# Optimization experiments

Measured on AMD Instinct MI355X. Metric: run time of the kernel, lower is better.

Reference implementation:

```python
import jax, jax.numpy as jnp
import numpy as np

STRIDE = 1
PAD = 1
KH = KW = 3


def _conv2d(x, w, b, stride, pad):
    out = jax.lax.conv_general_dilated(
        x, w, window_strides=(stride, stride),
        padding=[(pad, pad), (pad, pad)],
        dimension_numbers=("NCHW", "OIHW", "NCHW"))
    return out + b[None, :, None, None]


def _deform_conv2d(x, offset, mask, weight, stride, pad):
    """Modulated deformable conv v2 (torchvision deform_conv2d semantics, no bias).

    x: [B,C,H,W]  offset: [B,2*K2,Ho,Wo] (dy,dx interleaved per tap)
    mask: [B,K2,Ho,Wo]  weight: [O,C,KH,KW]
    """
    B, C, H, W = x.shape
    O = weight.shape[0]
    K2 = KH * KW
    Ho, Wo = offset.shape[2], offset.shape[3]

    dy = offset[:, 0::2]  # [B,K2,Ho,Wo]
    dx = offset[:, 1::2]

    # base sampling grid per kernel tap k = i*KW + j
    ki = jnp.repeat(jnp.arange(KH), KW)  # [K2]
    kj = jnp.tile(jnp.arange(KW), KH)    # [K2]
    base_y = (jnp.arange(Ho) * stride - pad)[None, :, None] + ki[:, None, None]  # [K2,Ho,1]
    base_x = (jnp.arange(Wo) * stride - pad)[None, None, :] + kj[:, None, None]  # [K2,1,Wo]

    py = base_y[None].astype(x.dtype) + dy  # [B,K2,Ho,Wo]
    px = base_x[None].astype(x.dtype) + dx

    y0f = jnp.floor(py)
    x0f = jnp.floor(px)
    wy = py - y0f  # bilinear weights
    wx = px - x0f
    y0 = y0f.astype(jnp.int32)
    x0 = x0f.astype(jnp.int32)

    x_flat = x.reshape(B, C, H * W)

    def gather(yi, xi):
        # zero padding: out-of-range integer neighbors contribute 0
        valid = (yi >= 0) & (yi < H) & (xi >= 0) & (xi < W)
        idx = jnp.clip(yi, 0, H - 1) * W + jnp.clip(xi, 0, W - 1)  # [B,K2,Ho,Wo]
        g = jax.vmap(lambda xf, id_: xf[:, id_])(x_flat, idx)      # [B,C,K2,Ho,Wo]
        return g * valid[:, None].astype(x.dtype)

    v00 = gather(y0, x0)
    v01 = gather(y0, x0 + 1)
    v10 = gather(y0 + 1, x0)
    v11 = gather(y0 + 1, x0 + 1)

    wy_ = wy[:, None]  # [B,1,K2,Ho,Wo]
    wx_ = wx[:, None]
    val = (v00 * (1 - wy_) * (1 - wx_) + v01 * (1 - wy_) * wx_
           + v10 * wy_ * (1 - wx_) + v11 * wy_ * wx_)
    val = val * mask[:, None]

    # conv accumulation over (C, K2)
    return jnp.einsum("bckhw,ock->bohw", val, weight.reshape(O, C, K2))


def setup_inputs() -> dict:
    key = jax.random.key(0)
    ks = jax.random.split(key, 6)
    B, C, O, H, W = 4, 128, 128, 64, 64
    x = jax.random.normal(ks[0], (B, C, H, W), dtype=jnp.float32)
    org_w = jax.random.normal(ks[1], (O, C, KH, KW), dtype=jnp.float32) * 0.05
    offset_w = jax.random.normal(ks[2], (2 * KH * KW, C, 3, 3), dtype=jnp.float32) * 0.01
    offset_b = jax.random.normal(ks[3], (2 * KH * KW,), dtype=jnp.float32) * 0.01
    mask_w = jax.random.normal(ks[4], (KH * KW, C, 3, 3), dtype=jnp.float32) * 0.01
    mask_b = jax.random.normal(ks[5], (KH * KW,), dtype=jnp.float32) * 0.01
    return {"x": x, "org_w": org_w, "offset_w": offset_w, "offset_b": offset_b,
            "mask_w": mask_w, "mask_b": mask_b}


def reference(x, org_w, offset_w, offset_b, mask_w, mask_b):
    offset = _conv2d(x, offset_w, offset_b, STRIDE, 1)          # [B,18,H,W]
    mask = jax.nn.sigmoid(_conv2d(x, mask_w, mask_b, STRIDE, 1))  # [B,9,H,W]
    return _deform_conv2d(x, offset, mask, org_w, STRIDE, PAD)
```

## Files before the change

kernel.cpp:

```cpp
#include <hip/hip_runtime.h>
#include <hip/hip_bf16.h>
#include <cmath>

#define B_    4
#define C_    128
#define O_    128
#define K2T   9
#define CK    1152
#define NPIX  4096
#define ROWS  8
#define BUFC  512
#define BUFF  8192
#define NGRP  36

using bf16   = __bf16;
using bf16x8 = __attribute__((ext_vector_type(8))) __bf16;
using f32x4  = __attribute__((ext_vector_type(4))) float;

#define WS_WBF 0
#define WS_WOM 294912

__global__ void __launch_bounds__(256) repack_kernel(
    const float* __restrict__ org_w, const float* __restrict__ offset_w,
    const float* __restrict__ mask_w, bf16* __restrict__ w_bf,
    bf16* __restrict__ wom_bf) {
  int t = blockIdx.x * 256 + threadIdx.x;
  if (t >= 160 * CK) return;
  int row = t / CK, r = t % CK;
  int cc = r / 288, rr = r % 288;
  int k = rr >> 5, cq = rr & 31;
  int c = cc * 32 + cq;
  if (row < 128) {
    w_bf[t] = (bf16)org_w[((size_t)row * C_ + c) * K2T + k];
  } else {
    int ch = row - 128;
    float v = 0.f;
    if (ch < 18)      v = offset_w[((size_t)ch * C_ + c) * K2T + k];
    else if (ch < 27) v = mask_w[((size_t)(ch - 18) * C_ + c) * K2T + k];
    wom_bf[(size_t)ch * CK + r] = (bf16)v;
  }
}

__device__ __forceinline__ void gl_lds16(const float* src, float* lds_uniform) {
  __builtin_amdgcn_global_load_lds(
      (const __attribute__((address_space(1))) void*)src,
      (__attribute__((address_space(3))) void*)lds_uniform, 16, 0, 0);
}

__global__ void __launch_bounds__(576) deform_fused_kernel(
    const float* __restrict__ x, const bf16* __restrict__ w_bf,
    const bf16* __restrict__ wom_bf, const float* __restrict__ off_b,
    const float* __restrict__ mask_b, float* __restrict__ out) {
  __shared__ __align__(16) float xslab[3 * BUFF];
  __shared__ __align__(16) bf16  valbuf[NGRP * 512];
  __shared__ __align__(16) float S_lds[32 * 64];

  int tid  = threadIdx.x;
  int bid0 = blockIdx.x;
  int bid  = (bid0 & 7) * 32 + (bid0 >> 3);
  int b    = bid >> 6, ho = bid & 63;
  int lane = tid & 63, wv = tid >> 6;
  int l15  = lane & 15, l4 = lane >> 4;
  bool w8  = (wv < 8);

  const float* xb = x + (size_t)b * C_ * NPIX;

  auto stage = [&](int it2) {
    if (w8 && it2 < 16) {
      int ccs = (it2 & 7) >> 1, g2s = it2 & 1;
      float* dstb = xslab + (it2 % 3) * BUFF;
#pragma unroll
      for (int u = 0; u < 2; ++u) {
        int chl = 2 * wv + u;
        int ch  = ccs * 32 + g2s * 16 + chl;
        const float* srcb = xb + (size_t)ch * NPIX + l15 * 4;
        float* dst = dstb + chl * BUFC;
#pragma unroll
        for (int j = 0; j < 2; ++j) {
          int y = ho - 3 + j * 4 + l4;
          y = y < 0 ? 0 : (y > 63 ? 63 : y);
          gl_lds16(srcb + y * 64, dst + j * 256);
        }
      }
    }
  };

  float apw; int apsa;
  {
    int k = wv, p = lane;
    int ki = k / 3, kj = k % 3;
    int row = ho - 1 + ki, colu = p - 1 + kj;
    bool ok = ((unsigned)row < 64u) && ((unsigned)colu < 64u);
    int cc0 = colu < 0 ? 0 : (colu > 63 ? 63 : colu);
    apw  = ok ? 1.f : 0.f;
    apsa = (ki + 2) * 64 + cc0;
  }

  stage(0);
  stage(1);
  __builtin_amdgcn_sched_barrier(0);

  f32x4 acc1 = {};
  f32x4 acc[4] = {};
  bf16x8 aF[9];
  float pw0 = 0.f, pw1 = 0.f, pw2 = 0.f, pw3 = 0.f;
  int   psa = 0, psb = 0;
  int   mf = wv & 1, nfq = wv >> 1;
  const bf16* wbase1 = wom_bf + (size_t)(mf * 16 + l15) * CK + l4 * 8;
  const bf16* wbase  = w_bf  + (size_t)(wv * 16 + l15) * CK + l4 * 8;
  const bf16* vb1    = valbuf + l4 * 512 + (nfq * 16 + l15) * 8;
  const bf16* vbase  = valbuf + l4 * 512 + l15 * 8;

#pragma unroll 1
  for (int hp = 0; hp < 16; ++hp) {
    int c2 = hp >> 1;
    bool passB = (c2 >= 4);
    int cc = c2 & 3;
    if (hp == 15) asm volatile("s_waitcnt vmcnt(0)" ::: "memory");
    else          asm volatile("s_waitcnt vmcnt(4)" ::: "memory");
    __builtin_amdgcn_s_barrier();
    __builtin_amdgcn_sched_barrier(0);
    if (!(hp & 1) && w8) {
      const bf16* ab = (passB ? wbase : wbase1) + cc * 288;
#pragma unroll
      for (int ks = 0; ks < 9; ++ks) aF[ks] = *(const bf16x8*)(ab + ks * 32);
      __builtin_amdgcn_sched_barrier(0);
    }
    stage(hp + 2);
    __builtin_amdgcn_sched_barrier(0);
    {
      const float* sbuf = xslab + (hp % 3) * BUFF;
      int grp = wv * 4 + (hp & 1) * 2;
      if (passB) {
#pragma unroll
        for (int h = 0; h < 2; ++h) {
          bf16x8 pack;
#pragma unroll
          for (int j = 0; j < 8; ++j) {
            const float* cb = sbuf + (h * 8 + j) * BUFC;
            float a0 = cb[psa], a1 = cb[psa + 64];
            float b0 = cb[psb], b1 = cb[psb + 64];
            pack[j] = (bf16)(pw0 * a0 + pw1 * b0 + pw2 * a1 + pw3 * b1);
          }
          *(bf16x8*)(valbuf + (grp + h) * 512 + lane * 8) = pack;
        }
      } else {
#pragma unroll
        for (int h = 0; h < 2; ++h) {
          bf16x8 pack;
#pragma unroll
          for (int j = 0; j < 8; ++j)
            pack[j] = (bf16)(apw * sbuf[(h * 8 + j) * BUFC + apsa]);
          *(bf16x8*)(valbuf + (grp + h) * 512 + lane * 8) = pack;
        }
      }
    }
    if (hp & 1) {
      asm volatile("s_waitcnt lgkmcnt(0)" ::: "memory");
      __builtin_amdgcn_s_barrier();
      __builtin_amdgcn_sched_barrier(0);
      if (w8) {
        __builtin_amdgcn_s_setprio(1);
        if (passB) {
#pragma unroll
          for (int ks = 0; ks < 9; ++ks) {
#pragma unroll
            for (int nf = 0; nf < 4; ++nf) {
              bf16x8 bv = *(const bf16x8*)(vbase + ks * 2048 + nf * 128);
              acc[nf] = __builtin_amdgcn_mfma_f32_16x16x32_bf16(aF[ks], bv, acc[nf], 0, 0, 0);
            }
          }
        } else {
#pragma unroll
          for (int ks = 0; ks < 9; ++ks) {
            bf16x8 bv = *(const bf16x8*)(vb1 + ks * 2048);
            acc1 = __builtin_amdgcn_mfma_f32_16x16x32_bf16(aF[ks], bv, acc1, 0, 0, 0);
          }
        }
        __builtin_amdgcn_s_setprio(0);
      }
    }
    if (hp == 7) {
      if (w8) {
        int so = mf * 16 + l4 * 4;
        int sp = nfq * 16 + l15;
#pragma unroll
        for (int r = 0; r < 4; ++r) S_lds[(so + r) * 64 + sp] = acc1[r];
      }
      asm volatile("s_waitcnt lgkmcnt(0)" ::: "memory");
      __builtin_amdgcn_s_barrier();
      __builtin_amdgcn_sched_barrier(0);
      {
        int k = wv, p = lane;
        float dy = S_lds[(2 * k) * 64 + p]     + off_b[2 * k];
        float dx = S_lds[(2 * k + 1) * 64 + p] + off_b[2 * k + 1];
        float mz = S_lds[(18 + k) * 64 + p]    + mask_b[k];
        float m  = 1.f / (1.f + expf(-mz));
        int ki = k / 3, kj = k % 3;
        float py = (float)(ho - 1 + ki) + dy;
        float px = (float)(p  - 1 + kj) + dx;
        float fy = floorf(py), fx = floorf(px);
        int y0 = (int)fy, x0 = (int)fx;
        float wy = py - fy, wx = px - fx;
        float vy0 = ((unsigned)y0       < 64u) ? 1.f : 0.f;
        float vy1 = ((unsigned)(y0 + 1) < 64u) ? 1.f : 0.f;
        float vx0 = ((unsigned)x0       < 64u) ? 1.f : 0.f;
        float vx1 = ((unsigned)(x0 + 1) < 64u) ? 1.f : 0.f;
        int r0  = y0 - (ho - 3);
        int ir0 = r0 < 0 ? 0 : (r0 > ROWS - 2 ? ROWS - 2 : r0);
        int c0  = x0 < 0 ? 0 : (x0 > 63 ? 63 : x0);
        int x1  = x0 + 1;
        int c1  = x1 < 0 ? 0 : (x1 > 63 ? 63 : x1);
        pw0 = (1.f - wy) * (1.f - wx) * m * vy0 * vx0;
        pw1 = (1.f - wy) * wx         * m * vy0 * vx1;
        pw2 = wy * (1.f - wx)         * m * vy1 * vx0;
        pw3 = wy * wx                 * m * vy1 * vx1;
        psa = ir0 * 64 + c0;
        psb = ir0 * 64 + c1;
      }
    }
  }

  if (w8) {
    float* ob = out + (size_t)b * O_ * NPIX + ho * 64;
#pragma unroll
    for (int nf = 0; nf < 4; ++nf)
#pragma unroll
      for (int r = 0; r < 4; ++r) {
        int o = wv * 16 + l4 * 4 + r;
        int p = nf * 16 + l15;
        ob[(size_t)o * NPIX + p] = acc[nf][r];
      }
  }
}

extern "C" void kernel_launch(void* const* d_in, const int* in_sizes, int n_in,
                              void* d_out, int out_size, void* d_ws, size_t ws_size,
                              hipStream_t stream) {
  const float* x        = (const float*)d_in[0];
  const float* org_w    = (const float*)d_in[1];
  const float* offset_w = (const float*)d_in[2];
  const float* off_b    = (const float*)d_in[3];
  const float* mask_w   = (const float*)d_in[4];
  const float* mask_b   = (const float*)d_in[5];
  float* out = (float*)d_out;
  char*  ws  = (char*)d_ws;

  bf16* w_bf   = (bf16*)(ws + WS_WBF);
  bf16* wom_bf = (bf16*)(ws + WS_WOM);

  repack_kernel<<<720, 256, 0, stream>>>(org_w, offset_w, mask_w, w_bf, wom_bf);
  deform_fused_kernel<<<256, 576, 0, stream>>>(x, w_bf, wom_bf, off_b, mask_b, out);
}
```

Before: 45.93 us.

## Widen fused deform kernel to 16 waves and redistribute sampling and MFMA work

Raises the block from 9 to 16 waves. All waves now stage x rows, share bilinear sampling work at quarter-channel granularity, and split the main GEMM so each wave owns half the pixel tiles. The offset/mask GEMM is split across two wave groups by even and odd k-steps, with the partial sums added through a doubled S_lds. LDS channel stride is padded to 516 to reduce bank conflicts. The aim is more latency hiding and more parallel gather throughput per CU, at the cost of more registers per wave, uneven per-thread sampling counts, and more barrier participants.

```diff
diff --git a/kernel.cpp b/kernel.cpp
--- a/kernel.cpp
+++ b/kernel.cpp
@@ -9,11 +9,12 @@
 #define CK    1152
 #define NPIX  4096
 #define ROWS  8
-#define BUFC  512
-#define BUFF  8192
+#define BUFC  516
+#define BUFF  (16 * BUFC)
 #define NGRP  36
 
 using bf16   = __bf16;
+using bf16x4 = __attribute__((ext_vector_type(4))) __bf16;
 using bf16x8 = __attribute__((ext_vector_type(8))) __bf16;
 using f32x4  = __attribute__((ext_vector_type(4))) float;
 
@@ -47,13 +48,13 @@
       (__attribute__((address_space(3))) void*)lds_uniform, 16, 0, 0);
 }
 
-__global__ void __launch_bounds__(576) deform_fused_kernel(
+__global__ void __launch_bounds__(1024) deform_fused_kernel(
     const float* __restrict__ x, const bf16* __restrict__ w_bf,
     const bf16* __restrict__ wom_bf, const float* __restrict__ off_b,
     const float* __restrict__ mask_b, float* __restrict__ out) {
   __shared__ __align__(16) float xslab[3 * BUFF];
   __shared__ __align__(16) bf16  valbuf[NGRP * 512];
-  __shared__ __align__(16) float S_lds[32 * 64];
+  __shared__ __align__(16) float S_lds[2 * 2048];
 
   int tid  = threadIdx.x;
   int bid0 = blockIdx.x;
@@ -61,39 +62,46 @@
   int b    = bid >> 6, ho = bid & 63;
   int lane = tid & 63, wv = tid >> 6;
   int l15  = lane & 15, l4 = lane >> 4;
-  bool w8  = (wv < 8);
 
   const float* xb = x + (size_t)b * C_ * NPIX;
 
   auto stage = [&](int it2) {
-    if (w8 && it2 < 16) {
+    if (it2 < 16) {
       int ccs = (it2 & 7) >> 1, g2s = it2 & 1;
-      float* dstb = xslab + (it2 % 3) * BUFF;
-#pragma unroll
-      for (int u = 0; u < 2; ++u) {
-        int chl = 2 * wv + u;
-        int ch  = ccs * 32 + g2s * 16 + chl;
-        const float* srcb = xb + (size_t)ch * NPIX + l15 * 4;
-        float* dst = dstb + chl * BUFC;
-#pragma unroll
-        for (int j = 0; j < 2; ++j) {
-          int y = ho - 3 + j * 4 + l4;
-          y = y < 0 ? 0 : (y > 63 ? 63 : y);
-          gl_lds16(srcb + y * 64, dst + j * 256);
-        }
+      int ch = ccs * 32 + g2s * 16 + wv;
+      float* dst = xslab + (it2 % 3) * BUFF + wv * BUFC;
+      const float* srcb = xb + (size_t)ch * NPIX + l15 * 4;
+#pragma unroll
+      for (int j = 0; j < 2; ++j) {
+        int y = ho - 3 + j * 4 + l4;
+        y = y < 0 ? 0 : (y > 63 ? 63 : y);
+        gl_lds16(srcb + y * 64, dst + j * 256);
       }
     }
   };
 
-  float apw; int apsa;
+  int nu = ((tid & 3) == 0) ? 3 : 2;
+  int ku[3], pu[3], qu[3];
   {
-    int k = wv, p = lane;
+    int us0 = tid, us1 = tid + 1024, us2 = 2048 + (tid >> 2);
+    int uu[3] = {us0, us1, us2};
+#pragma unroll
+    for (int i = 0; i < 3; ++i) {
+      ku[i] = uu[i] >> 8;
+      int rem = uu[i] & 255;
+      pu[i] = rem >> 2; qu[i] = rem & 3;
+    }
+  }
+  float apw[3]; int apsa[3];
+#pragma unroll
+  for (int i = 0; i < 3; ++i) {
+    int k = ku[i], p = pu[i];
     int ki = k / 3, kj = k % 3;
     int row = ho - 1 + ki, colu = p - 1 + kj;
     bool ok = ((unsigned)row < 64u) && ((unsigned)colu < 64u);
-    int cc0 = colu < 0 ? 0 : (colu > 63 ? 63 : colu);
-    apw  = ok ? 1.f : 0.f;
-    apsa = (ki + 2) * 64 + cc0;
+    int ccl = colu < 0 ? 0 : (colu > 63 ? 63 : colu);
+    apw[i]  = ok ? 1.f : 0.f;
+    apsa[i] = (ki + 2) * 64 + ccl;
   }
 
   stage(0);
@@ -101,27 +109,30 @@
   __builtin_amdgcn_sched_barrier(0);
 
   f32x4 acc1 = {};
-  f32x4 acc[4] = {};
+  f32x4 acc[2] = {};
   bf16x8 aF[9];
-  float pw0 = 0.f, pw1 = 0.f, pw2 = 0.f, pw3 = 0.f;
-  int   psa = 0, psb = 0;
-  int   mf = wv & 1, nfq = wv >> 1;
-  const bf16* wbase1 = wom_bf + (size_t)(mf * 16 + l15) * CK + l4 * 8;
-  const bf16* wbase  = w_bf  + (size_t)(wv * 16 + l15) * CK + l4 * 8;
-  const bf16* vb1    = valbuf + l4 * 512 + (nfq * 16 + l15) * 8;
-  const bf16* vbase  = valbuf + l4 * 512 + l15 * 8;
+  float pw[3][4]; int psa[3] = {0, 0, 0}, psb[3] = {0, 0, 0};
+#pragma unroll
+  for (int i = 0; i < 3; ++i) { pw[i][0] = pw[i][1] = pw[i][2] = pw[i][3] = 0.f; }
+  int g = wv >> 3, w8i = wv & 7;
+  int mf1 = w8i & 1, nfq1 = w8i >> 1;
+  int mt = wv >> 1, npr = wv & 1;
+  const bf16* wb1 = wom_bf + (size_t)(mf1 * 16 + l15) * CK + l4 * 8;
+  const bf16* wb  = w_bf  + (size_t)(mt * 16 + l15) * CK + l4 * 8;
+  const bf16* vr1 = valbuf + l4 * 512 + (nfq1 * 16 + l15) * 8;
+  const bf16* vrB = valbuf + l4 * 512 + l15 * 8;
 
 #pragma unroll 1
   for (int hp = 0; hp < 16; ++hp) {
-    int c2 = hp >> 1;
-    bool passB = (c2 >= 4);
-    int cc = c2 & 3;
-    if (hp == 15) asm volatile("s_waitcnt vmcnt(0)" ::: "memory");
-    else          asm volatile("s_waitcnt vmcnt(4)" ::: "memory");
+    bool passB = (hp >= 8);
+    int cc = (hp >> 1) & 3;
+    if (hp == 15)     asm volatile("s_waitcnt vmcnt(0)" ::: "memory");
+    else if (hp & 1)  asm volatile("s_waitcnt vmcnt(11)" ::: "memory");
+    else              asm volatile("s_waitcnt vmcnt(2)" ::: "memory");
     __builtin_amdgcn_s_barrier();
     __builtin_amdgcn_sched_barrier(0);
-    if (!(hp & 1) && w8) {
-      const bf16* ab = (passB ? wbase : wbase1) + cc * 288;
+    if (!(hp & 1)) {
+      const bf16* ab = (passB ? wb : wb1) + cc * 288;
 #pragma unroll
       for (int ks = 0; ks < 9; ++ks) aF[ks] = *(const bf16x8*)(ab + ks * 32);
       __builtin_amdgcn_sched_barrier(0);
@@ -130,28 +141,29 @@
     __builtin_amdgcn_sched_barrier(0);
     {
       const float* sbuf = xslab + (hp % 3) * BUFF;
-      int grp = wv * 4 + (hp & 1) * 2;
-      if (passB) {
-#pragma unroll
-        for (int h = 0; h < 2; ++h) {
-          bf16x8 pack;
-#pragma unroll
-          for (int j = 0; j < 8; ++j) {
-            const float* cb = sbuf + (h * 8 + j) * BUFC;
-            float a0 = cb[psa], a1 = cb[psa + 64];
-            float b0 = cb[psb], b1 = cb[psb + 64];
-            pack[j] = (bf16)(pw0 * a0 + pw1 * b0 + pw2 * a1 + pw3 * b1);
-          }
-          *(bf16x8*)(valbuf + (grp + h) * 512 + lane * 8) = pack;
-        }
-      } else {
-#pragma unroll
-        for (int h = 0; h < 2; ++h) {
-          bf16x8 pack;
-#pragma unroll
-          for (int j = 0; j < 8; ++j)
-            pack[j] = (bf16)(apw * sbuf[(h * 8 + j) * BUFC + apsa]);
-          *(bf16x8*)(valbuf + (grp + h) * 512 + lane * 8) = pack;
+      int gb = (hp & 1) * 2;
+#pragma unroll
+      for (int i = 0; i < 3; ++i) {
+        if (i < nu) {
+          bf16x4 pk4;
+          if (passB) {
+#pragma unroll
+            for (int j = 0; j < 4; ++j) {
+              const float* cb = sbuf + (qu[i] * 4 + j) * BUFC;
+              float a0 = cb[psa[i]], a1 = cb[psa[i] + 64];
+              float b0 = cb[psb[i]], b1 = cb[psb[i] + 64];
+              pk4[j] = (bf16)(pw[i][0] * a0 + pw[i][1] * b0 +
+                              pw[i][2] * a1 + pw[i][3] * b1);
+            }
+          } else {
+#pragma unroll
+            for (int j = 0; j < 4; ++j) {
+              const float* cb = sbuf + (qu[i] * 4 + j) * BUFC;
+              pk4[j] = (bf16)(apw[i] * cb[apsa[i]]);
+            }
+          }
+          *(bf16x4*)(valbuf + (ku[i] * 4 + gb + (qu[i] >> 1)) * 512 +
+                     pu[i] * 8 + (qu[i] & 1) * 4) = pk4;
         }
       }
     }
@@ -159,76 +171,85 @@
       asm volatile("s_waitcnt lgkmcnt(0)" ::: "memory");
       __builtin_amdgcn_s_barrier();
       __builtin_amdgcn_sched_barrier(0);
-      if (w8) {
+      if (passB) {
         __builtin_amdgcn_s_setprio(1);
-        if (passB) {
-#pragma unroll
-          for (int ks = 0; ks < 9; ++ks) {
-#pragma unroll
-            for (int nf = 0; nf < 4; ++nf) {
-              bf16x8 bv = *(const bf16x8*)(vbase + ks * 2048 + nf * 128);
-              acc[nf] = __builtin_amdgcn_mfma_f32_16x16x32_bf16(aF[ks], bv, acc[nf], 0, 0, 0);
-            }
+#pragma unroll
+        for (int ks = 0; ks < 9; ++ks) {
+#pragma unroll
+          for (int nf = 0; nf < 2; ++nf) {
+            bf16x8 bv = *(const bf16x8*)(vrB + ks * 2048 + (npr * 2 + nf) * 128);
+            acc[nf] = __builtin_amdgcn_mfma_f32_16x16x32_bf16(aF[ks], bv, acc[nf], 0, 0, 0);
+          }
+        }
+        __builtin_amdgcn_s_setprio(0);
+      } else {
+        if (g == 0) {
+#pragma unroll
+          for (int ksi = 0; ksi < 5; ++ksi) {
+            bf16x8 bv = *(const bf16x8*)(vr1 + (2 * ksi) * 2048);
+            acc1 = __builtin_amdgcn_mfma_f32_16x16x32_bf16(aF[2 * ksi], bv, acc1, 0, 0, 0);
           }
         } else {
 #pragma unroll
-          for (int ks = 0; ks < 9; ++ks) {
-            bf16x8 bv = *(const bf16x8*)(vb1 + ks * 2048);
-            acc1 = __builtin_amdgcn_mfma_f32_16x16x32_bf16(aF[ks], bv, acc1, 0, 0, 0);
-          }
-        }
-        __builtin_amdgcn_s_setprio(0);
+          for (int ksi = 0; ksi < 4; ++ksi) {
+            bf16x8 bv = *(const bf16x8*)(vr1 + (2 * ksi + 1) * 2048);
+            acc1 = __builtin_amdgcn_mfma_f32_16x16x32_bf16(aF[2 * ksi + 1], bv, acc1, 0, 0, 0);
+          }
+        }
       }
     }
     if (hp == 7) {
-      if (w8) {
-        int so = mf * 16 + l4 * 4;
-        int sp = nfq * 16 + l15;
-#pragma unroll
-        for (int r = 0; r < 4; ++r) S_lds[(so + r) * 64 + sp] = acc1[r];
+      {
+        int so = mf1 * 16 + l4 * 4;
+        int sp = nfq1 * 16 + l15;
+#pragma unroll
+        for (int r = 0; r < 4; ++r) S_lds[g * 2048 + (so + r) * 64 + sp] = acc1[r];
       }
       asm volatile("s_waitcnt lgkmcnt(0)" ::: "memory");
       __builtin_amdgcn_s_barrier();
       __builtin_amdgcn_sched_barrier(0);
-      {
-        int k = wv, p = lane;
-        float dy = S_lds[(2 * k) * 64 + p]     + off_b[2 * k];
-        float dx = S_lds[(2 * k + 1) * 64 + p] + off_b[2 * k + 1];
-        float mz = S_lds[(18 + k) * 64 + p]    + mask_b[k];
-        float m  = 1.f / (1.f + expf(-mz));
-        int ki = k / 3, kj = k % 3;
-        float py = (float)(ho - 1 + ki) + dy;
-        float px = (float)(p  - 1 + kj) + dx;
-        float fy = floorf(py), fx = floorf(px);
-        int y0 = (int)fy, x0 = (int)fx;
-        float wy = py - fy, wx = px - fx;
-        float vy0 = ((unsigned)y0       < 64u) ? 1.f : 0.f;
-        float vy1 = ((unsigned)(y0 + 1) < 64u) ? 1.f : 0.f;
-        float vx0 = ((unsigned)x0       < 64u) ? 1.f : 0.f;
-        float vx1 = ((unsigned)(x0 + 1) < 64u) ? 1.f : 0.f;
-        int r0  = y0 - (ho - 3);
-        int ir0 = r0 < 0 ? 0 : (r0 > ROWS - 2 ? ROWS - 2 : r0);
-        int c0  = x0 < 0 ? 0 : (x0 > 63 ? 63 : x0);
-        int x1  = x0 + 1;
-        int c1  = x1 < 0 ? 0 : (x1 > 63 ? 63 : x1);
-        pw0 = (1.f - wy) * (1.f - wx) * m * vy0 * vx0;
-        pw1 = (1.f - wy) * wx         * m * vy0 * vx1;
-        pw2 = wy * (1.f - wx)         * m * vy1 * vx0;
-        pw3 = wy * wx                 * m * vy1 * vx1;
-        psa = ir0 * 64 + c0;
-        psb = ir0 * 64 + c1;
-      }
-    }
-  }
-
-  if (w8) {
+#pragma unroll
+      for (int i = 0; i < 3; ++i) {
+        if (i < nu) {
+          int k = ku[i], p = pu[i];
+          float dy = S_lds[(2 * k) * 64 + p]     + S_lds[2048 + (2 * k) * 64 + p]     + off_b[2 * k];
+          float dx = S_lds[(2 * k + 1) * 64 + p] + S_lds[2048 + (2 * k + 1) * 64 + p] + off_b[2 * k + 1];
+          float mz = S_lds[(18 + k) * 64 + p]    + S_lds[2048 + (18 + k) * 64 + p]    + mask_b[k];
+          float m  = 1.f / (1.f + expf(-mz));
+          int ki = k / 3, kj = k % 3;
+          float py = (float)(ho - 1 + ki) + dy;
+          float px = (float)(p  - 1 + kj) + dx;
+          float fy = floorf(py), fx = floorf(px);
+          int y0 = (int)fy, x0 = (int)fx;
+          float wy = py - fy, wx = px - fx;
+          float vy0 = ((unsigned)y0       < 64u) ? 1.f : 0.f;
+          float vy1 = ((unsigned)(y0 + 1) < 64u) ? 1.f : 0.f;
+          float vx0 = ((unsigned)x0       < 64u) ? 1.f : 0.f;
+          float vx1 = ((unsigned)(x0 + 1) < 64u) ? 1.f : 0.f;
+          int r0  = y0 - (ho - 3);
+          int ir0 = r0 < 0 ? 0 : (r0 > ROWS - 2 ? ROWS - 2 : r0);
+          int c0  = x0 < 0 ? 0 : (x0 > 63 ? 63 : x0);
+          int x1  = x0 + 1;
+          int c1  = x1 < 0 ? 0 : (x1 > 63 ? 63 : x1);
+          pw[i][0] = (1.f - wy) * (1.f - wx) * m * vy0 * vx0;
+          pw[i][1] = (1.f - wy) * wx         * m * vy0 * vx1;
+          pw[i][2] = wy * (1.f - wx)         * m * vy1 * vx0;
+          pw[i][3] = wy * wx                 * m * vy1 * vx1;
+          psa[i] = ir0 * 64 + c0;
+          psb[i] = ir0 * 64 + c1;
+        }
+      }
+    }
+  }
+
+  {
     float* ob = out + (size_t)b * O_ * NPIX + ho * 64;
 #pragma unroll
-    for (int nf = 0; nf < 4; ++nf)
+    for (int nf = 0; nf < 2; ++nf)
 #pragma unroll
       for (int r = 0; r < 4; ++r) {
-        int o = wv * 16 + l4 * 4 + r;
-        int p = nf * 16 + l15;
+        int o = mt * 16 + l4 * 4 + r;
+        int p = (npr * 2 + nf) * 16 + l15;
         ob[(size_t)o * NPIX + p] = acc[nf][r];
       }
   }
@@ -250,5 +271,5 @@
   bf16* wom_bf = (bf16*)(ws + WS_WOM);
 
   repack_kernel<<<720, 256, 0, stream>>>(org_w, offset_w, mask_w, w_bf, wom_bf);
-  deform_fused_kernel<<<256, 576, 0, stream>>>(x, w_bf, wom_bf, off_b, mask_b, out);
-}
+  deform_fused_kernel<<<256, 1024, 0, stream>>>(x, w_bf, wom_bf, off_b, mask_b, out);
+}
```

Measured after the change: 73.12 us. +59.2%, slower.

## Split fused deform kernel into param, split-K deform, and reduce kernels

Applied to the files above, without the earlier changes.

Replaces the single fused kernel, which computed the offset/mask conv and then the deformable conv per output row, with three kernels. The first computes the offset/mask conv and stores per-tap bilinear weights (as fp16) and packed indices in workspace. The second runs the deformable conv over 512 blocks, each covering half the channels, and writes partial sums. The third adds the two halves. The aim is more parallelism and a smaller LDS footprint for higher occupancy, at the cost of extra launches, a 16 MB partials round trip through global memory, and fp16 rounding of the bilinear weights.

```diff
diff --git a/kernel.cpp b/kernel.cpp
--- a/kernel.cpp
+++ b/kernel.cpp
@@ -8,17 +8,17 @@
 #define K2T   9
 #define CK    1152
 #define NPIX  4096
-#define ROWS  8
-#define BUFC  512
-#define BUFF  8192
-#define NGRP  36
 
 using bf16   = __bf16;
 using bf16x8 = __attribute__((ext_vector_type(8))) __bf16;
 using f32x4  = __attribute__((ext_vector_type(4))) float;
 
-#define WS_WBF 0
-#define WS_WOM 294912
+#define WS_WBF  0
+#define WS_WOM  294912
+#define WS_PWH  368640
+#define WS_PO   1548288
+#define WS_PART 2138112
+#define HALF_ELEMS 2097152
 
 __global__ void __launch_bounds__(256) repack_kernel(
     const float* __restrict__ org_w, const float* __restrict__ offset_w,
@@ -47,12 +47,12 @@
       (__attribute__((address_space(3))) void*)lds_uniform, 16, 0, 0);
 }
 
-__global__ void __launch_bounds__(576) deform_fused_kernel(
-    const float* __restrict__ x, const bf16* __restrict__ w_bf,
-    const bf16* __restrict__ wom_bf, const float* __restrict__ off_b,
-    const float* __restrict__ mask_b, float* __restrict__ out) {
-  __shared__ __align__(16) float xslab[3 * BUFF];
-  __shared__ __align__(16) bf16  valbuf[NGRP * 512];
+__global__ void __launch_bounds__(576) offmask_params_kernel(
+    const float* __restrict__ x, const bf16* __restrict__ wom_bf,
+    const float* __restrict__ off_b, const float* __restrict__ mask_b,
+    uint2* __restrict__ pwh, int* __restrict__ po_) {
+  __shared__ __align__(16) float xslab[3 * 4096];
+  __shared__ __align__(16) bf16  valbuf[36 * 512];
   __shared__ __align__(16) float S_lds[32 * 64];
 
   int tid  = threadIdx.x;
@@ -66,34 +66,27 @@
   const float* xb = x + (size_t)b * C_ * NPIX;
 
   auto stage = [&](int it2) {
-    if (w8 && it2 < 16) {
-      int ccs = (it2 & 7) >> 1, g2s = it2 & 1;
-      float* dstb = xslab + (it2 % 3) * BUFF;
+    if (w8 && it2 < 8) {
+      float* dstb = xslab + (it2 % 3) * 4096;
+      int y = ho - 1 + l4;
+      y = y < 0 ? 0 : (y > 63 ? 63 : y);
 #pragma unroll
       for (int u = 0; u < 2; ++u) {
         int chl = 2 * wv + u;
-        int ch  = ccs * 32 + g2s * 16 + chl;
-        const float* srcb = xb + (size_t)ch * NPIX + l15 * 4;
-        float* dst = dstb + chl * BUFC;
-#pragma unroll
-        for (int j = 0; j < 2; ++j) {
-          int y = ho - 3 + j * 4 + l4;
-          y = y < 0 ? 0 : (y > 63 ? 63 : y);
-          gl_lds16(srcb + y * 64, dst + j * 256);
-        }
+        int ch  = it2 * 16 + chl;
+        gl_lds16(xb + (size_t)ch * NPIX + y * 64 + l15 * 4, dstb + chl * 256);
       }
     }
   };
 
   float apw; int apsa;
   {
-    int k = wv, p = lane;
-    int ki = k / 3, kj = k % 3;
-    int row = ho - 1 + ki, colu = p - 1 + kj;
+    int ki = wv / 3, kj = wv % 3;
+    int row = ho - 1 + ki, colu = lane - 1 + kj;
     bool ok = ((unsigned)row < 64u) && ((unsigned)colu < 64u);
-    int cc0 = colu < 0 ? 0 : (colu > 63 ? 63 : colu);
+    int ccl = colu < 0 ? 0 : (colu > 63 ? 63 : colu);
     apw  = ok ? 1.f : 0.f;
-    apsa = (ki + 2) * 64 + cc0;
+    apsa = ki * 64 + ccl;
   }
 
   stage(0);
@@ -101,27 +94,19 @@
   __builtin_amdgcn_sched_barrier(0);
 
   f32x4 acc1 = {};
-  f32x4 acc[4] = {};
   bf16x8 aF[9];
-  float pw0 = 0.f, pw1 = 0.f, pw2 = 0.f, pw3 = 0.f;
-  int   psa = 0, psb = 0;
-  int   mf = wv & 1, nfq = wv >> 1;
-  const bf16* wbase1 = wom_bf + (size_t)(mf * 16 + l15) * CK + l4 * 8;
-  const bf16* wbase  = w_bf  + (size_t)(wv * 16 + l15) * CK + l4 * 8;
-  const bf16* vb1    = valbuf + l4 * 512 + (nfq * 16 + l15) * 8;
-  const bf16* vbase  = valbuf + l4 * 512 + l15 * 8;
+  int mf1 = wv & 1, nfq1 = wv >> 1;
+  const bf16* wb1 = wom_bf + (size_t)(mf1 * 16 + l15) * CK + l4 * 8;
+  const bf16* vr1 = valbuf + l4 * 512 + (nfq1 * 16 + l15) * 8;
 
 #pragma unroll 1
-  for (int hp = 0; hp < 16; ++hp) {
-    int c2 = hp >> 1;
-    bool passB = (c2 >= 4);
-    int cc = c2 & 3;
-    if (hp == 15) asm volatile("s_waitcnt vmcnt(0)" ::: "memory");
-    else          asm volatile("s_waitcnt vmcnt(4)" ::: "memory");
+  for (int hp = 0; hp < 8; ++hp) {
+    if (hp == 7) asm volatile("s_waitcnt vmcnt(0)" ::: "memory");
+    else         asm volatile("s_waitcnt vmcnt(2)" ::: "memory");
     __builtin_amdgcn_s_barrier();
     __builtin_amdgcn_sched_barrier(0);
     if (!(hp & 1) && w8) {
-      const bf16* ab = (passB ? wbase : wbase1) + cc * 288;
+      const bf16* ab = wb1 + (hp >> 1) * 288;
 #pragma unroll
       for (int ks = 0; ks < 9; ++ks) aF[ks] = *(const bf16x8*)(ab + ks * 32);
       __builtin_amdgcn_sched_barrier(0);
@@ -129,30 +114,15 @@
     stage(hp + 2);
     __builtin_amdgcn_sched_barrier(0);
     {
-      const float* sbuf = xslab + (hp % 3) * BUFF;
-      int grp = wv * 4 + (hp & 1) * 2;
-      if (passB) {
-#pragma unroll
-        for (int h = 0; h < 2; ++h) {
-          bf16x8 pack;
-#pragma unroll
-          for (int j = 0; j < 8; ++j) {
-            const float* cb = sbuf + (h * 8 + j) * BUFC;
-            float a0 = cb[psa], a1 = cb[psa + 64];
-            float b0 = cb[psb], b1 = cb[psb + 64];
-            pack[j] = (bf16)(pw0 * a0 + pw1 * b0 + pw2 * a1 + pw3 * b1);
-          }
-          *(bf16x8*)(valbuf + (grp + h) * 512 + lane * 8) = pack;
-        }
-      } else {
-#pragma unroll
-        for (int h = 0; h < 2; ++h) {
-          bf16x8 pack;
-#pragma unroll
-          for (int j = 0; j < 8; ++j)
-            pack[j] = (bf16)(apw * sbuf[(h * 8 + j) * BUFC + apsa]);
-          *(bf16x8*)(valbuf + (grp + h) * 512 + lane * 8) = pack;
-        }
+      const float* sbuf = xslab + (hp % 3) * 4096;
+      int gb = (hp & 1) * 2;
+#pragma unroll
+      for (int h = 0; h < 2; ++h) {
+        bf16x8 pack;
+#pragma unroll
+        for (int j = 0; j < 8; ++j)
+          pack[j] = (bf16)(apw * sbuf[(h * 8 + j) * 256 + apsa]);
+        *(bf16x8*)(valbuf + (wv * 4 + gb + h) * 512 + lane * 8) = pack;
       }
     }
     if (hp & 1) {
@@ -161,68 +131,153 @@
       __builtin_amdgcn_sched_barrier(0);
       if (w8) {
         __builtin_amdgcn_s_setprio(1);
-        if (passB) {
-#pragma unroll
-          for (int ks = 0; ks < 9; ++ks) {
-#pragma unroll
-            for (int nf = 0; nf < 4; ++nf) {
-              bf16x8 bv = *(const bf16x8*)(vbase + ks * 2048 + nf * 128);
-              acc[nf] = __builtin_amdgcn_mfma_f32_16x16x32_bf16(aF[ks], bv, acc[nf], 0, 0, 0);
-            }
-          }
-        } else {
-#pragma unroll
-          for (int ks = 0; ks < 9; ++ks) {
-            bf16x8 bv = *(const bf16x8*)(vb1 + ks * 2048);
-            acc1 = __builtin_amdgcn_mfma_f32_16x16x32_bf16(aF[ks], bv, acc1, 0, 0, 0);
+#pragma unroll
+        for (int ks = 0; ks < 9; ++ks) {
+          bf16x8 bv = *(const bf16x8*)(vr1 + ks * 2048);
+          acc1 = __builtin_amdgcn_mfma_f32_16x16x32_bf16(aF[ks], bv, acc1, 0, 0, 0);
+        }
+        __builtin_amdgcn_s_setprio(0);
+      }
+    }
+  }
+
+  if (w8) {
+    int so = mf1 * 16 + l4 * 4;
+    int sp = nfq1 * 16 + l15;
+#pragma unroll
+    for (int r = 0; r < 4; ++r) S_lds[(so + r) * 64 + sp] = acc1[r];
+  }
+  asm volatile("s_waitcnt lgkmcnt(0)" ::: "memory");
+  __builtin_amdgcn_s_barrier();
+  __builtin_amdgcn_sched_barrier(0);
+  {
+    int k = wv, p = lane;
+    float dy = S_lds[(2 * k) * 64 + p]     + off_b[2 * k];
+    float dx = S_lds[(2 * k + 1) * 64 + p] + off_b[2 * k + 1];
+    float mz = S_lds[(18 + k) * 64 + p]    + mask_b[k];
+    float m  = 1.f / (1.f + expf(-mz));
+    int ki = k / 3, kj = k % 3;
+    float py = (float)(ho - 1 + ki) + dy;
+    float px = (float)(p  - 1 + kj) + dx;
+    float fy = floorf(py), fx = floorf(px);
+    int y0 = (int)fy, x0 = (int)fx;
+    float wy = py - fy, wx = px - fx;
+    float vy0 = ((unsigned)y0       < 64u) ? 1.f : 0.f;
+    float vy1 = ((unsigned)(y0 + 1) < 64u) ? 1.f : 0.f;
+    float vx0 = ((unsigned)x0       < 64u) ? 1.f : 0.f;
+    float vx1 = ((unsigned)(x0 + 1) < 64u) ? 1.f : 0.f;
+    int r0  = y0 - (ho - 3);
+    int ir0 = r0 < 0 ? 0 : (r0 > 6 ? 6 : r0);
+    int c0  = x0 < 0 ? 0 : (x0 > 63 ? 63 : x0);
+    int x1  = x0 + 1;
+    int c1  = x1 < 0 ? 0 : (x1 > 63 ? 63 : x1);
+    float pw0 = (1.f - wy) * (1.f - wx) * m * vy0 * vx0;
+    float pw1 = (1.f - wy) * wx         * m * vy0 * vx1;
+    float pw2 = wy * (1.f - wx)         * m * vy1 * vx0;
+    float pw3 = wy * wx                 * m * vy1 * vx1;
+    int psa = ir0 * 64 + c0;
+    int psb = ir0 * 64 + c1;
+    unsigned short h0 = __builtin_bit_cast(unsigned short, (_Float16)pw0);
+    unsigned short h1 = __builtin_bit_cast(unsigned short, (_Float16)pw1);
+    unsigned short h2 = __builtin_bit_cast(unsigned short, (_Float16)pw2);
+    unsigned short h3 = __builtin_bit_cast(unsigned short, (_Float16)pw3);
+    int idx = ((b * 9 + k) << 12) + ho * 64 + p;
+    pwh[idx] = make_uint2((unsigned)h0 | ((unsigned)h1 << 16),
+                          (unsigned)h2 | ((unsigned)h3 << 16));
+    po_[idx] = psa | (psb << 9);
+  }
+}
+
+__global__ void __launch_bounds__(576, 5) deform_kernel(
+    const float* __restrict__ x, const bf16* __restrict__ w_bf,
+    const uint2* __restrict__ pwh, const int* __restrict__ po_,
+    float* __restrict__ partials) {
+  __shared__ __align__(16) float xslab[2 * 4096];
+  __shared__ __align__(16) bf16  valbuf[36 * 512];
+
+  int tid  = threadIdx.x;
+  int bid0 = blockIdx.x;
+  int bid  = (bid0 & 7) * 64 + (bid0 >> 3);
+  int b    = bid >> 7;
+  int rem  = bid & 127;
+  int ho   = rem >> 1, kh = rem & 1;
+  int lane = tid & 63, wv = tid >> 6;
+  int l15  = lane & 15, l4 = lane >> 4;
+  bool w8  = (wv < 8);
+
+  const float* xb = x + (size_t)b * C_ * NPIX;
+
+  auto stage = [&](int hp2) {
+    if (w8 && hp2 < 8) {
+      int ch = (kh * 2 + (hp2 >> 2)) * 32 + (hp2 & 3) * 8 + wv;
+      float* dst = xslab + (hp2 & 1) * 4096 + wv * 512;
+      const float* srcb = xb + (size_t)ch * NPIX + l15 * 4;
+#pragma unroll
+      for (int j = 0; j < 2; ++j) {
+        int y = ho - 3 + j * 4 + l4;
+        y = y < 0 ? 0 : (y > 63 ? 63 : y);
+        gl_lds16(srcb + y * 64, dst + j * 256);
+      }
+    }
+  };
+
+  int idx = ((b * 9 + wv) << 12) + ho * 64 + lane;
+  uint2 hp4 = pwh[idx];
+  int   pp  = po_[idx];
+  stage(0);
+  float pw0 = (float)__builtin_bit_cast(_Float16, (unsigned short)(hp4.x & 0xFFFF));
+  float pw1 = (float)__builtin_bit_cast(_Float16, (unsigned short)(hp4.x >> 16));
+  float pw2 = (float)__builtin_bit_cast(_Float16, (unsigned short)(hp4.y & 0xFFFF));
+  float pw3 = (float)__builtin_bit_cast(_Float16, (unsigned short)(hp4.y >> 16));
+  int psa = pp & 511, psb = (pp >> 9) & 511;
+
+  f32x4 acc[4] = {};
+  const bf16* wb  = w_bf + (size_t)(wv * 16 + l15) * CK + l4 * 8;
+  const bf16* vrB = valbuf + l4 * 512 + l15 * 8;
+
+#pragma unroll 1
+  for (int hp = 0; hp < 8; ++hp) {
+    int g = hp & 3;
+    asm volatile("s_waitcnt vmcnt(0)" ::: "memory");
+    __builtin_amdgcn_s_barrier();
+    __builtin_amdgcn_sched_barrier(0);
+    stage(hp + 1);
+    __builtin_amdgcn_sched_barrier(0);
+    {
+      const float* sbuf = xslab + (hp & 1) * 4096;
+      bf16x8 pack;
+#pragma unroll
+      for (int j = 0; j < 8; ++j) {
+        const float* cb = sbuf + j * 512;
+        float a0 = cb[psa], a1 = cb[psa + 64];
+        float b0 = cb[psb], b1 = cb[psb + 64];
+        pack[j] = (bf16)(pw0 * a0 + pw1 * b0 + pw2 * a1 + pw3 * b1);
+      }
+      *(bf16x8*)(valbuf + (wv * 4 + g) * 512 + lane * 8) = pack;
+    }
+    if (g == 3) {
+      asm volatile("s_waitcnt lgkmcnt(0)" ::: "memory");
+      __builtin_amdgcn_s_barrier();
+      __builtin_amdgcn_sched_barrier(0);
+      if (w8) {
+        const bf16* ab = wb + (kh * 2 + (hp >> 2)) * 288;
+        __builtin_amdgcn_s_setprio(1);
+#pragma unroll
+        for (int ks = 0; ks < 9; ++ks) {
+          bf16x8 af = *(const bf16x8*)(ab + ks * 32);
+#pragma unroll
+          for (int nf = 0; nf < 4; ++nf) {
+            bf16x8 bv = *(const bf16x8*)(vrB + ks * 2048 + nf * 128);
+            acc[nf] = __builtin_amdgcn_mfma_f32_16x16x32_bf16(af, bv, acc[nf], 0, 0, 0);
           }
         }
         __builtin_amdgcn_s_setprio(0);
       }
     }
-    if (hp == 7) {
-      if (w8) {
-        int so = mf * 16 + l4 * 4;
-        int sp = nfq * 16 + l15;
-#pragma unroll
-        for (int r = 0; r < 4; ++r) S_lds[(so + r) * 64 + sp] = acc1[r];
-      }
-      asm volatile("s_waitcnt lgkmcnt(0)" ::: "memory");
-      __builtin_amdgcn_s_barrier();
-      __builtin_amdgcn_sched_barrier(0);
-      {
-        int k = wv, p = lane;
-        float dy = S_lds[(2 * k) * 64 + p]     + off_b[2 * k];
-        float dx = S_lds[(2 * k + 1) * 64 + p] + off_b[2 * k + 1];
-        float mz = S_lds[(18 + k) * 64 + p]    + mask_b[k];
-        float m  = 1.f / (1.f + expf(-mz));
-        int ki = k / 3, kj = k % 3;
-        float py = (float)(ho - 1 + ki) + dy;
-        float px = (float)(p  - 1 + kj) + dx;
-        float fy = floorf(py), fx = floorf(px);
-        int y0 = (int)fy, x0 = (int)fx;
-        float wy = py - fy, wx = px - fx;
-        float vy0 = ((unsigned)y0       < 64u) ? 1.f : 0.f;
-        float vy1 = ((unsigned)(y0 + 1) < 64u) ? 1.f : 0.f;
-        float vx0 = ((unsigned)x0       < 64u) ? 1.f : 0.f;
-        float vx1 = ((unsigned)(x0 + 1) < 64u) ? 1.f : 0.f;
-        int r0  = y0 - (ho - 3);
-        int ir0 = r0 < 0 ? 0 : (r0 > ROWS - 2 ? ROWS - 2 : r0);
-        int c0  = x0 < 0 ? 0 : (x0 > 63 ? 63 : x0);
-        int x1  = x0 + 1;
-        int c1  = x1 < 0 ? 0 : (x1 > 63 ? 63 : x1);
-        pw0 = (1.f - wy) * (1.f - wx) * m * vy0 * vx0;
-        pw1 = (1.f - wy) * wx         * m * vy0 * vx1;
-        pw2 = wy * (1.f - wx)         * m * vy1 * vx0;
-        pw3 = wy * wx                 * m * vy1 * vx1;
-        psa = ir0 * 64 + c0;
-        psb = ir0 * 64 + c1;
-      }
-    }
   }
 
   if (w8) {
-    float* ob = out + (size_t)b * O_ * NPIX + ho * 64;
+    float* ob = partials + (size_t)kh * HALF_ELEMS + (size_t)b * O_ * NPIX + ho * 64;
 #pragma unroll
     for (int nf = 0; nf < 4; ++nf)
 #pragma unroll
@@ -232,6 +287,16 @@
         ob[(size_t)o * NPIX + p] = acc[nf][r];
       }
   }
+}
+
+__global__ void __launch_bounds__(256) reduce_kernel(
+    const float* __restrict__ partials, float* __restrict__ out) {
+  int t = blockIdx.x * 256 + threadIdx.x;
+  const float4* p0 = (const float4*)partials;
+  const float4* p1 = (const float4*)(partials + HALF_ELEMS);
+  float4 a = p0[t], c = p1[t];
+  float4 r = make_float4(a.x + c.x, a.y + c.y, a.z + c.z, a.w + c.w);
+  ((float4*)out)[t] = r;
 }
 
 extern "C" void kernel_launch(void* const* d_in, const int* in_sizes, int n_in,
@@ -246,9 +311,14 @@
   float* out = (float*)d_out;
   char*  ws  = (char*)d_ws;
 
-  bf16* w_bf   = (bf16*)(ws + WS_WBF);
-  bf16* wom_bf = (bf16*)(ws + WS_WOM);
+  bf16*  w_bf     = (bf16*)(ws + WS_WBF);
+  bf16*  wom_bf   = (bf16*)(ws + WS_WOM);
+  uint2* pwh      = (uint2*)(ws + WS_PWH);
+  int*   po_      = (int*)(ws + WS_PO);
+  float* partials = (float*)(ws + WS_PART);
 
   repack_kernel<<<720, 256, 0, stream>>>(org_w, offset_w, mask_w, w_bf, wom_bf);
-  deform_fused_kernel<<<256, 576, 0, stream>>>(x, w_bf, wom_bf, off_b, mask_b, out);
-}
+  offmask_params_kernel<<<256, 576, 0, stream>>>(x, wom_bf, off_b, mask_b, pwh, po_);
+  deform_kernel<<<512, 576, 0, stream>>>(x, w_bf, pwh, po_, partials);
+  reduce_kernel<<<2048, 256, 0, stream>>>(partials, out);
+}
```

New measurement: 55.93 us. +21.8%, slower.

## Restructure x staging into 8 double-chunk passes with a 4-deep slab ring

Applied to the files above, without the earlier changes.

The main loop now does 8 passes of 32 channels instead of 16 half-passes, so it has fewer barriers and waitcnt points. It keeps a 4-buffer ring of 7-row x slabs and issues the next two stages right after the barrier that frees their buffers. The offset/mask pass now loads only the 4 rows it needs instead of 8, which cuts global-to-LDS traffic. The cost is a deeper vmcnt schedule that has to match per-stage load counts, and a slightly different LDS footprint.

```diff
diff --git a/kernel.cpp b/kernel.cpp
--- a/kernel.cpp
+++ b/kernel.cpp
@@ -8,9 +8,9 @@
 #define K2T   9
 #define CK    1152
 #define NPIX  4096
-#define ROWS  8
-#define BUFC  512
-#define BUFF  8192
+#define ROWS  7
+#define BUFC  448
+#define BUFV  (16 * BUFC)
 #define NGRP  36
 
 using bf16   = __bf16;
@@ -51,7 +51,7 @@
     const float* __restrict__ x, const bf16* __restrict__ w_bf,
     const bf16* __restrict__ wom_bf, const float* __restrict__ off_b,
     const float* __restrict__ mask_b, float* __restrict__ out) {
-  __shared__ __align__(16) float xslab[3 * BUFF];
+  __shared__ __align__(16) float xslab[4 * BUFV];
   __shared__ __align__(16) bf16  valbuf[NGRP * 512];
   __shared__ __align__(16) float S_lds[32 * 64];
 
@@ -65,21 +65,23 @@
 
   const float* xb = x + (size_t)b * C_ * NPIX;
 
-  auto stage = [&](int it2) {
-    if (w8 && it2 < 16) {
-      int ccs = (it2 & 7) >> 1, g2s = it2 & 1;
-      float* dstb = xslab + (it2 % 3) * BUFF;
+  auto stage = [&](int t) {
+    if (w8 && t < 16) {
+      int chbase = (t & 7) * 16;
+      float* bufb = xslab + (size_t)(t & 3) * BUFV;
 #pragma unroll
       for (int u = 0; u < 2; ++u) {
         int chl = 2 * wv + u;
-        int ch  = ccs * 32 + g2s * 16 + chl;
-        const float* srcb = xb + (size_t)ch * NPIX + l15 * 4;
-        float* dst = dstb + chl * BUFC;
-#pragma unroll
-        for (int j = 0; j < 2; ++j) {
-          int y = ho - 3 + j * 4 + l4;
-          y = y < 0 ? 0 : (y > 63 ? 63 : y);
-          gl_lds16(srcb + y * 64, dst + j * 256);
+        const float* srcc = xb + (size_t)(chbase + chl) * NPIX + l15 * 4;
+        float* dst = bufb + chl * BUFC;
+        if (t < 8) {
+          int y = ho - 1 + l4; y = y < 0 ? 0 : (y > 63 ? 63 : y);
+          gl_lds16(srcc + y * 64, dst + 128);
+        } else {
+          int ya = ho - 3 + l4; ya = ya < 0 ? 0 : (ya > 63 ? 63 : ya);
+          int yb = ho + l4;     yb = yb < 0 ? 0 : (yb > 63 ? 63 : yb);
+          gl_lds16(srcc + ya * 64, dst);
+          gl_lds16(srcc + yb * 64, dst + 192);
         }
       }
     }
@@ -87,17 +89,15 @@
 
   float apw; int apsa;
   {
-    int k = wv, p = lane;
-    int ki = k / 3, kj = k % 3;
-    int row = ho - 1 + ki, colu = p - 1 + kj;
+    int ki = wv / 3, kj = wv % 3;
+    int row = ho - 1 + ki, colu = lane - 1 + kj;
     bool ok = ((unsigned)row < 64u) && ((unsigned)colu < 64u);
-    int cc0 = colu < 0 ? 0 : (colu > 63 ? 63 : colu);
+    int ccl = colu < 0 ? 0 : (colu > 63 ? 63 : colu);
     apw  = ok ? 1.f : 0.f;
-    apsa = (ki + 2) * 64 + cc0;
-  }
-
-  stage(0);
-  stage(1);
+    apsa = (ki + 2) * 64 + ccl;
+  }
+
+  stage(0); stage(1); stage(2); stage(3);
   __builtin_amdgcn_sched_barrier(0);
 
   f32x4 acc1 = {};
@@ -105,85 +105,80 @@
   bf16x8 aF[9];
   float pw0 = 0.f, pw1 = 0.f, pw2 = 0.f, pw3 = 0.f;
   int   psa = 0, psb = 0;
-  int   mf = wv & 1, nfq = wv >> 1;
-  const bf16* wbase1 = wom_bf + (size_t)(mf * 16 + l15) * CK + l4 * 8;
-  const bf16* wbase  = w_bf  + (size_t)(wv * 16 + l15) * CK + l4 * 8;
-  const bf16* vb1    = valbuf + l4 * 512 + (nfq * 16 + l15) * 8;
-  const bf16* vbase  = valbuf + l4 * 512 + l15 * 8;
+  int   mf1 = wv & 1, nfq1 = wv >> 1;
+  const bf16* wb1 = wom_bf + (size_t)(mf1 * 16 + l15) * CK + l4 * 8;
+  const bf16* wb  = w_bf  + (size_t)(wv * 16 + l15) * CK + l4 * 8;
+  const bf16* vr1 = valbuf + l4 * 512 + (nfq1 * 16 + l15) * 8;
+  const bf16* vrB = valbuf + l4 * 512 + l15 * 8;
 
 #pragma unroll 1
-  for (int hp = 0; hp < 16; ++hp) {
-    int c2 = hp >> 1;
-    bool passB = (c2 >= 4);
-    int cc = c2 & 3;
-    if (hp == 15) asm volatile("s_waitcnt vmcnt(0)" ::: "memory");
-    else          asm volatile("s_waitcnt vmcnt(4)" ::: "memory");
+  for (int p = 0; p < 8; ++p) {
+    bool passB = (p >= 4);
+    int cc = p & 3;
+    if (p == 7)      asm volatile("s_waitcnt vmcnt(0)" ::: "memory");
+    else if (p < 3)  asm volatile("s_waitcnt vmcnt(4)" ::: "memory");
+    else             asm volatile("s_waitcnt vmcnt(8)" ::: "memory");
     __builtin_amdgcn_s_barrier();
     __builtin_amdgcn_sched_barrier(0);
-    if (!(hp & 1) && w8) {
-      const bf16* ab = (passB ? wbase : wbase1) + cc * 288;
+    if (w8) {
+      const bf16* ab = (passB ? wb : wb1) + cc * 288;
 #pragma unroll
       for (int ks = 0; ks < 9; ++ks) aF[ks] = *(const bf16x8*)(ab + ks * 32);
       __builtin_amdgcn_sched_barrier(0);
     }
-    stage(hp + 2);
-    __builtin_amdgcn_sched_barrier(0);
     {
-      const float* sbuf = xslab + (hp % 3) * BUFF;
-      int grp = wv * 4 + (hp & 1) * 2;
-      if (passB) {
-#pragma unroll
-        for (int h = 0; h < 2; ++h) {
-          bf16x8 pack;
+      const float* bufA = xslab + (size_t)((2 * p) & 3) * BUFV;
+      const float* bufB2 = xslab + (size_t)((2 * p + 1) & 3) * BUFV;
+#pragma unroll
+      for (int q = 0; q < 4; ++q) {
+        const float* bb = (q < 2) ? bufA : bufB2;
+        int h = q & 1;
+        bf16x8 pack;
+        if (passB) {
 #pragma unroll
           for (int j = 0; j < 8; ++j) {
-            const float* cb = sbuf + (h * 8 + j) * BUFC;
+            const float* cb = bb + (h * 8 + j) * BUFC;
             float a0 = cb[psa], a1 = cb[psa + 64];
             float b0 = cb[psb], b1 = cb[psb + 64];
             pack[j] = (bf16)(pw0 * a0 + pw1 * b0 + pw2 * a1 + pw3 * b1);
           }
-          *(bf16x8*)(valbuf + (grp + h) * 512 + lane * 8) = pack;
+        } else {
+#pragma unroll
+          for (int j = 0; j < 8; ++j)
+            pack[j] = (bf16)(apw * bb[(h * 8 + j) * BUFC + apsa]);
+        }
+        *(bf16x8*)(valbuf + (wv * 4 + q) * 512 + lane * 8) = pack;
+      }
+    }
+    asm volatile("s_waitcnt lgkmcnt(0)" ::: "memory");
+    __builtin_amdgcn_s_barrier();
+    __builtin_amdgcn_sched_barrier(0);
+    stage(2 * p + 4); stage(2 * p + 5);
+    __builtin_amdgcn_sched_barrier(0);
+    if (w8) {
+      __builtin_amdgcn_s_setprio(1);
+      if (passB) {
+#pragma unroll
+        for (int ks = 0; ks < 9; ++ks) {
+#pragma unroll
+          for (int nf = 0; nf < 4; ++nf) {
+            bf16x8 bv = *(const bf16x8*)(vrB + ks * 2048 + nf * 128);
+            acc[nf] = __builtin_amdgcn_mfma_f32_16x16x32_bf16(aF[ks], bv, acc[nf], 0, 0, 0);
+          }
         }
       } else {
 #pragma unroll
-        for (int h = 0; h < 2; ++h) {
-          bf16x8 pack;
-#pragma unroll
-          for (int j = 0; j < 8; ++j)
-            pack[j] = (bf16)(apw * sbuf[(h * 8 + j) * BUFC + apsa]);
-          *(bf16x8*)(valbuf + (grp + h) * 512 + lane * 8) = pack;
-        }
-      }
-    }
-    if (hp & 1) {
-      asm volatile("s_waitcnt lgkmcnt(0)" ::: "memory");
-      __builtin_amdgcn_s_barrier();
-      __builtin_amdgcn_sched_barrier(0);
+        for (int ks = 0; ks < 9; ++ks) {
+          bf16x8 bv = *(const bf16x8*)(vr1 + ks * 2048);
+          acc1 = __builtin_amdgcn_mfma_f32_16x16x32_bf16(aF[ks], bv, acc1, 0, 0, 0);
+        }
+      }
+      __builtin_amdgcn_s_setprio(0);
+    }
+    if (p == 3) {
       if (w8) {
-        __builtin_amdgcn_s_setprio(1);
-        if (passB) {
-#pragma unroll
-          for (int ks = 0; ks < 9; ++ks) {
-#pragma unroll
-            for (int nf = 0; nf < 4; ++nf) {
-              bf16x8 bv = *(const bf16x8*)(vbase + ks * 2048 + nf * 128);
-              acc[nf] = __builtin_amdgcn_mfma_f32_16x16x32_bf16(aF[ks], bv, acc[nf], 0, 0, 0);
-            }
-          }
-        } else {
-#pragma unroll
-          for (int ks = 0; ks < 9; ++ks) {
-            bf16x8 bv = *(const bf16x8*)(vb1 + ks * 2048);
-            acc1 = __builtin_amdgcn_mfma_f32_16x16x32_bf16(aF[ks], bv, acc1, 0, 0, 0);
-          }
-        }
-        __builtin_amdgcn_s_setprio(0);
-      }
-    }
-    if (hp == 7) {
-      if (w8) {
-        int so = mf * 16 + l4 * 4;
-        int sp = nfq * 16 + l15;
+        int so = mf1 * 16 + l4 * 4;
+        int sp = nfq1 * 16 + l15;
 #pragma unroll
         for (int r = 0; r < 4; ++r) S_lds[(so + r) * 64 + sp] = acc1[r];
       }
@@ -191,14 +186,14 @@
       __builtin_amdgcn_s_barrier();
       __builtin_amdgcn_sched_barrier(0);
       {
-        int k = wv, p = lane;
-        float dy = S_lds[(2 * k) * 64 + p]     + off_b[2 * k];
-        float dx = S_lds[(2 * k + 1) * 64 + p] + off_b[2 * k + 1];
-        float mz = S_lds[(18 + k) * 64 + p]    + mask_b[k];
+        int k = wv, pp = lane;
+        float dy = S_lds[(2 * k) * 64 + pp]     + off_b[2 * k];
+        float dx = S_lds[(2 * k + 1) * 64 + pp] + off_b[2 * k + 1];
+        float mz = S_lds[(18 + k) * 64 + pp]    + mask_b[k];
         float m  = 1.f / (1.f + expf(-mz));
         int ki = k / 3, kj = k % 3;
         float py = (float)(ho - 1 + ki) + dy;
-        float px = (float)(p  - 1 + kj) + dx;
+        float px = (float)(pp - 1 + kj) + dx;
         float fy = floorf(py), fx = floorf(px);
         int y0 = (int)fy, x0 = (int)fx;
         float wy = py - fy, wx = px - fx;
@@ -228,8 +223,8 @@
 #pragma unroll
       for (int r = 0; r < 4; ++r) {
         int o = wv * 16 + l4 * 4 + r;
-        int p = nf * 16 + l15;
-        ob[(size_t)o * NPIX + p] = acc[nf][r];
+        int pp = nf * 16 + l15;
+        ob[(size_t)o * NPIX + pp] = acc[nf][r];
       }
   }
 }
```

New measurement: 41.40 us. 1.11x faster.
